# Kernel tuning notes

Measured on AMD Instinct MI355X. Metric: run time of the kernel, lower is better.

## Reference

```python
import jax, jax.numpy as jnp
import numpy as np

N_NODES = 100000
N_EDGES = 3200000
D = 256


def setup_inputs() -> dict:
    key = jax.random.key(0)
    ks = jax.random.split(key, 8)
    ego_embeddings = jax.random.normal(ks[0], (N_NODES, D), dtype=jnp.float32) * 0.1
    edge_vals = jax.random.uniform(ks[1], (N_EDGES,), dtype=jnp.float32) / 32.0  # ~normalized adjacency
    W1 = jax.random.normal(ks[2], (D, D), dtype=jnp.float32) * (1.0 / np.sqrt(D))
    b1 = jnp.zeros((D,), dtype=jnp.float32)
    W2 = jax.random.normal(ks[3], (D, D), dtype=jnp.float32) * (1.0 / np.sqrt(D))
    b2 = jnp.zeros((D,), dtype=jnp.float32)
    edge_rows = jax.random.randint(ks[4], (N_EDGES,), 0, N_NODES, dtype=jnp.int32)
    edge_cols = jax.random.randint(ks[5], (N_EDGES,), 0, N_NODES, dtype=jnp.int32)
    return {"ego_embeddings": ego_embeddings, "edge_vals": edge_vals,
            "W1": W1, "b1": b1, "W2": W2, "b2": b2,
            "edge_rows": edge_rows, "edge_cols": edge_cols}


def reference(ego_embeddings, edge_vals, W1, b1, W2, b2, edge_rows, edge_cols):
    # SpMM: side = A_in @ ego  (A_in in COO: rows, cols, vals)
    n = ego_embeddings.shape[0]
    gathered = ego_embeddings[edge_cols] * edge_vals[:, None]      # [E, D]
    side = jax.ops.segment_sum(gathered, edge_rows, num_segments=n)  # [N, D]
    # bi-interaction aggregator
    sum_emb = jax.nn.leaky_relu((ego_embeddings + side) @ W1.T + b1, negative_slope=0.01)
    bi_emb = jax.nn.leaky_relu((ego_embeddings * side) @ W2.T + b2, negative_slope=0.01)
    # dropout p=0.0 -> identity
    return sum_emb + bi_emb
```

## Files before the change

### kernel.cpp

```cpp
#include <hip/hip_runtime.h>
#include <hip/hip_fp16.h>
#include <stdint.h>

#define D 256
#define CHSH 13

typedef __attribute__((ext_vector_type(8))) short short8;
typedef __attribute__((ext_vector_type(4))) float floatx4;

__device__ __forceinline__ ushort f2bf(float f) {
    union { float f; uint32_t u; } v; v.f = f;
    uint32_t u = v.u;
    u += 0x7fffu + ((u >> 16) & 1u);
    return (ushort)(u >> 16);
}
__device__ __forceinline__ float bf2f(ushort h) {
    union { uint32_t u; float f; } v; v.u = ((uint32_t)h) << 16;
    return v.f;
}


__global__ void k_hist(const int* __restrict__ er, const int* __restrict__ ec,
                       int* __restrict__ bp, int E, int NCH) {
    int e = blockIdx.x * 256 + threadIdx.x;
    if (e >= E) return;
    atomicAdd(&bp[er[e] * NCH + (ec[e] >> CHSH)], 1);
}

__global__ void k_red(const int* __restrict__ bp, int* __restrict__ part, int nb) {
    __shared__ int s[256];
    int t = threadIdx.x;
    int base = blockIdx.x * 1024 + t * 4;
    int v = 0;
#pragma unroll
    for (int j = 0; j < 4; ++j) if (base + j < nb) v += bp[base + j];
    s[t] = v; __syncthreads();
    for (int off = 128; off; off >>= 1) {
        if (t < off) s[t] += s[t + off];
        __syncthreads();
    }
    if (t == 0) part[blockIdx.x] = s[0];
}

__global__ __launch_bounds__(1024) void k_scanpart(int* __restrict__ part, int np) {
    __shared__ int s[1024];
    int t = threadIdx.x;
    int p0 = (2 * t < np) ? part[2 * t] : 0;
    int p1 = (2 * t + 1 < np) ? part[2 * t + 1] : 0;
    int v = p0 + p1;
    s[t] = v; __syncthreads();
    for (int off = 1; off < 1024; off <<= 1) {
        int x = (t >= off) ? s[t - off] : 0;
        __syncthreads();
        s[t] += x;
        __syncthreads();
    }
    int excl = s[t] - v;
    if (2 * t < np) part[2 * t] = excl;
    if (2 * t + 1 < np) part[2 * t + 1] = excl + p0;
}

__global__ void k_scan3(int* __restrict__ bp, const int* __restrict__ part, int nb) {
    __shared__ int s[256];
    int t = threadIdx.x;
    int base = blockIdx.x * 1024 + t * 4;
    int d0 = 0, d1 = 0, d2 = 0, d3 = 0;
    if (base     < nb) d0 = bp[base];
    if (base + 1 < nb) d1 = bp[base + 1];
    if (base + 2 < nb) d2 = bp[base + 2];
    if (base + 3 < nb) d3 = bp[base + 3];
    int sum = d0 + d1 + d2 + d3;
    s[t] = sum; __syncthreads();
    for (int off = 1; off < 256; off <<= 1) {
        int x = (t >= off) ? s[t - off] : 0;
        __syncthreads();
        s[t] += x;
        __syncthreads();
    }
    int run = part[blockIdx.x] + s[t] - sum;
    if (base     < nb) bp[base]     = run; run += d0;
    if (base + 1 < nb) bp[base + 1] = run; run += d1;
    if (base + 2 < nb) bp[base + 2] = run; run += d2;
    if (base + 3 < nb) bp[base + 3] = run;
}

__global__ void k_scatter(const int* __restrict__ er, const int* __restrict__ ec,
                          const float* __restrict__ ev, int* __restrict__ bp,
                          uint32_t* __restrict__ csr, int E, int NCH) {
    int e = blockIdx.x * 256 + threadIdx.x;
    if (e >= E) return;
    int col = ec[e];
    int p = atomicAdd(&bp[er[e] * NCH + (col >> CHSH)], 1);
    ushort hb = __half_as_ushort(__float2half_rn(ev[e]));
    csr[p] = ((uint32_t)col << 15) | (uint32_t)hb;
}

__global__ void k_cvt(const float4* __restrict__ ego, ushort4* __restrict__ ego_bf,
                      const float4* __restrict__ W1, const float4* __restrict__ W2,
                      ushort4* __restrict__ W1b, ushort4* __restrict__ W2b, int n4) {
    int i = blockIdx.x * 256 + threadIdx.x;
    const float4* src;
    ushort4* dst;
    if (i < n4) { src = ego + i; dst = ego_bf + i; }
    else {
        int j = i - n4;
        if (j >= 32768) return;
        int k = j & 16383;
        src = ((j < 16384) ? W1 : W2) + k;
        dst = ((j < 16384) ? W1b : W2b) + k;
    }
    float4 f = *src;
    ushort4 u;
    u.x = f2bf(f.x); u.y = f2bf(f.y); u.z = f2bf(f.z); u.w = f2bf(f.w);
    *dst = u;
}

__global__ void k_spmm(const ushort* __restrict__ ego_bf, const int* __restrict__ bp,
                       const uint32_t* __restrict__ csr,
                       ushort* __restrict__ X1, ushort* __restrict__ X2, int n, int NCH) {
    int gtid = blockIdx.x * 256 + threadIdx.x;
    int node = gtid >> 6;
    int lane = gtid & 63;
    if (node >= n) return;
    int beg = (node == 0) ? 0 : bp[node * NCH - 1];
    int end = bp[(node + 1) * NCH - 1];
    int d0 = lane * 4;
    float a0 = 0.f, a1 = 0.f, a2 = 0.f, a3 = 0.f;
    int e = beg;
    for (; e + 8 <= end; e += 8) {
        uint32_t w[8];
#pragma unroll
        for (int j = 0; j < 8; ++j) w[j] = csr[e + j];
        ushort4 u[8];
#pragma unroll
        for (int j = 0; j < 8; ++j)
            u[j] = *(const ushort4*)(ego_bf + (size_t)(w[j] >> 15) * D + d0);
#pragma unroll
        for (int j = 0; j < 8; ++j) {
            float v = __half2float(__ushort_as_half((ushort)(w[j] & 0x7fff)));
            a0 += v * bf2f(u[j].x);
            a1 += v * bf2f(u[j].y);
            a2 += v * bf2f(u[j].z);
            a3 += v * bf2f(u[j].w);
        }
    }
    for (; e < end; ++e) {
        uint32_t w = csr[e];
        float v = __half2float(__ushort_as_half((ushort)(w & 0x7fff)));
        ushort4 u = *(const ushort4*)(ego_bf + (size_t)(w >> 15) * D + d0);
        a0 += v * bf2f(u.x);
        a1 += v * bf2f(u.y);
        a2 += v * bf2f(u.z);
        a3 += v * bf2f(u.w);
    }
    ushort4 eg = *(const ushort4*)(ego_bf + (size_t)node * D + d0);
    float e0 = bf2f(eg.x), e1 = bf2f(eg.y), e2 = bf2f(eg.z), e3 = bf2f(eg.w);
    ushort4 o1, o2;
    o1.x = f2bf(e0 + a0); o2.x = f2bf(e0 * a0);
    o1.y = f2bf(e1 + a1); o2.y = f2bf(e1 * a1);
    o1.z = f2bf(e2 + a2); o2.z = f2bf(e2 * a2);
    o1.w = f2bf(e3 + a3); o2.w = f2bf(e3 * a3);
    *(ushort4*)(X1 + (size_t)node * D + d0) = o1;
    *(ushort4*)(X2 + (size_t)node * D + d0) = o2;
}

__global__ __launch_bounds__(256) void k_gemm(
        const ushort* __restrict__ X1, const ushort* __restrict__ X2,
        const ushort* __restrict__ W1b, const ushort* __restrict__ W2b,
        const float* __restrict__ b1, const float* __restrict__ b2,
        float* __restrict__ out, int n) {
    int lane = threadIdx.x & 63;
    int w = threadIdx.x >> 6;
    int l16 = lane & 15, quad = lane >> 4;
    int row0 = blockIdx.x * 64;
    int colw = w * 64;

    floatx4 acc1[4][4], acc2[4][4];
#pragma unroll
    for (int i = 0; i < 4; ++i)
#pragma unroll
        for (int j = 0; j < 4; ++j) { acc1[i][j] = (floatx4)0.f; acc2[i][j] = (floatx4)0.f; }

    for (int kk = 0; kk < D; kk += 32) {
        short8 a[4], b[4];
#pragma unroll
        for (int mt = 0; mt < 4; ++mt)
            a[mt] = *(const short8*)(X1 + (size_t)(row0 + mt * 16 + l16) * D + kk + quad * 8);
#pragma unroll
        for (int nt = 0; nt < 4; ++nt)
            b[nt] = *(const short8*)(W1b + (size_t)(colw + nt * 16 + l16) * D + kk + quad * 8);
#pragma unroll
        for (int mt = 0; mt < 4; ++mt)
#pragma unroll
            for (int nt = 0; nt < 4; ++nt)
                acc1[mt][nt] = __builtin_amdgcn_mfma_f32_16x16x32_bf16(a[mt], b[nt], acc1[mt][nt], 0, 0, 0);
    }
    for (int kk = 0; kk < D; kk += 32) {
        short8 a[4], b[4];
#pragma unroll
        for (int mt = 0; mt < 4; ++mt)
            a[mt] = *(const short8*)(X2 + (size_t)(row0 + mt * 16 + l16) * D + kk + quad * 8);
#pragma unroll
        for (int nt = 0; nt < 4; ++nt)
            b[nt] = *(const short8*)(W2b + (size_t)(colw + nt * 16 + l16) * D + kk + quad * 8);
#pragma unroll
        for (int mt = 0; mt < 4; ++mt)
#pragma unroll
            for (int nt = 0; nt < 4; ++nt)
                acc2[mt][nt] = __builtin_amdgcn_mfma_f32_16x16x32_bf16(a[mt], b[nt], acc2[mt][nt], 0, 0, 0);
    }

#pragma unroll
    for (int nt = 0; nt < 4; ++nt) {
        int col = colw + nt * 16 + l16;
        float bb1 = b1[col], bb2 = b2[col];
#pragma unroll
        for (int mt = 0; mt < 4; ++mt) {
            int row = row0 + mt * 16 + quad * 4;
#pragma unroll
            for (int r = 0; r < 4; ++r) {
                if (row + r < n) {
                    float v1 = acc1[mt][nt][r] + bb1;
                    v1 = v1 > 0.f ? v1 : 0.01f * v1;
                    float v2 = acc2[mt][nt][r] + bb2;
                    v2 = v2 > 0.f ? v2 : 0.01f * v2;
                    out[(size_t)(row + r) * D + col] = v1 + v2;
                }
            }
        }
    }
}

extern "C" void kernel_launch(void* const* d_in, const int* in_sizes, int n_in,
                              void* d_out, int out_size, void* d_ws, size_t ws_size,
                              hipStream_t stream) {
    const float* ego   = (const float*)d_in[0];
    const float* evals = (const float*)d_in[1];
    const float* W1    = (const float*)d_in[2];
    const float* b1    = (const float*)d_in[3];
    const float* W2    = (const float*)d_in[4];
    const float* b2    = (const float*)d_in[5];
    const int* erows   = (const int*)d_in[6];
    const int* ecols   = (const int*)d_in[7];
    float* out = (float*)d_out;

    int n = in_sizes[0] / D;
    int E = in_sizes[1];
    int npad = (n + 63) & ~63;
    int NCH = (n + (1 << CHSH) - 1) >> CHSH;
    int nb = n * NCH;
    int np = (nb + 1023) / 1024;

    char* p = (char*)d_ws;
    auto alloc = [&](size_t bytes) {
        char* q = p;
        p += (bytes + 511) & ~(size_t)511;
        return q;
    };
    ushort* ego_bf = (ushort*)alloc((size_t)n * D * 2);
    ushort* X1     = (ushort*)alloc((size_t)npad * D * 2);
    ushort* X2     = (ushort*)alloc((size_t)npad * D * 2);
    ushort* W1b    = (ushort*)alloc((size_t)D * D * 2);
    ushort* W2b    = (ushort*)alloc((size_t)D * D * 2);
    int* bp        = (int*)alloc((size_t)nb * 4);
    int* part      = (int*)alloc((size_t)np * 4);
    uint32_t* csr  = (uint32_t*)alloc((size_t)E * 4);

    hipMemsetAsync(bp, 0, (size_t)nb * 4, stream);
    k_hist<<<(E + 255) / 256, 256, 0, stream>>>(erows, ecols, bp, E, NCH);
    k_red<<<np, 256, 0, stream>>>(bp, part, nb);
    k_scanpart<<<1, 1024, 0, stream>>>(part, np);
    k_scan3<<<np, 256, 0, stream>>>(bp, part, nb);
    k_scatter<<<(E + 255) / 256, 256, 0, stream>>>(erows, ecols, evals, bp, csr, E, NCH);

    int n4 = n * (D / 4);
    k_cvt<<<(n4 + 32768 + 255) / 256, 256, 0, stream>>>((const float4*)ego, (ushort4*)ego_bf,
                                                        (const float4*)W1, (const float4*)W2,
                                                        (ushort4*)W1b, (ushort4*)W2b, n4);

    k_spmm<<<(n * 64 + 255) / 256, 256, 0, stream>>>(ego_bf, bp, csr, X1, X2, n, NCH);

    k_gemm<<<npad / 64, 256, 0, stream>>>(X1, X2, W1b, W2b, b1, b2, out, n);
}
```

Before: 893.2 us.

## Replace global fine-grained bucket sort with two-level 64-row bin sort for CSR

The CSR build no longer runs a global histogram plus a three-kernel scan over n*NCH buckets (about 1.3M counters). Edges are first binned into groups of 64 rows using a shared-memory histogram and a single-block scan. Each bin is then locally sorted by (row, column-chunk) in shared memory, which also produces the row pointers. This cuts global atomics contention and the large scan passes. In exchange it adds an 8-byte intermediate record pass, which reuses the X2 buffer as scratch, and the scan assumes at most 2048 bins.

```diff
diff --git a/kernel.cpp b/kernel.cpp
--- a/kernel.cpp
+++ b/kernel.cpp
@@ -20,33 +20,31 @@
 }
 
 
-__global__ void k_hist(const int* __restrict__ er, const int* __restrict__ ec,
-                       int* __restrict__ bp, int E, int NCH) {
-    int e = blockIdx.x * 256 + threadIdx.x;
-    if (e >= E) return;
-    atomicAdd(&bp[er[e] * NCH + (ec[e] >> CHSH)], 1);
-}
-
-__global__ void k_red(const int* __restrict__ bp, int* __restrict__ part, int nb) {
-    __shared__ int s[256];
+__global__ __launch_bounds__(1024) void k_hist0(const int* __restrict__ er,
+                                                int* __restrict__ cc, int E, int NB) {
+    __shared__ int h[2048];
     int t = threadIdx.x;
-    int base = blockIdx.x * 1024 + t * 4;
-    int v = 0;
-#pragma unroll
-    for (int j = 0; j < 4; ++j) if (base + j < nb) v += bp[base + j];
-    s[t] = v; __syncthreads();
-    for (int off = 128; off; off >>= 1) {
-        if (t < off) s[t] += s[t + off];
-        __syncthreads();
-    }
-    if (t == 0) part[blockIdx.x] = s[0];
-}
-
-__global__ __launch_bounds__(1024) void k_scanpart(int* __restrict__ part, int np) {
+    h[t] = 0; h[t + 1024] = 0;
+    __syncthreads();
+    int base = blockIdx.x * 32768;
+    for (int i = t; i < 32768; i += 1024) {
+        int e = base + i;
+        if (e < E) atomicAdd(&h[er[e] >> 6], 1);
+    }
+    __syncthreads();
+    int v = h[t];
+    if (t < NB && v) atomicAdd(&cc[t], v);
+    v = h[t + 1024];
+    if (t + 1024 < NB && v) atomicAdd(&cc[t + 1024], v);
+}
+
+__global__ __launch_bounds__(1024) void k_scan0(const int* __restrict__ cc,
+                                                int* __restrict__ cbase, int* __restrict__ cursor,
+                                                int* __restrict__ rowp, int NB, int E, int n) {
     __shared__ int s[1024];
     int t = threadIdx.x;
-    int p0 = (2 * t < np) ? part[2 * t] : 0;
-    int p1 = (2 * t + 1 < np) ? part[2 * t + 1] : 0;
+    int p0 = (2 * t < NB) ? cc[2 * t] : 0;
+    int p1 = (2 * t + 1 < NB) ? cc[2 * t + 1] : 0;
     int v = p0 + p1;
     s[t] = v; __syncthreads();
     for (int off = 1; off < 1024; off <<= 1) {
@@ -56,43 +54,60 @@
         __syncthreads();
     }
     int excl = s[t] - v;
-    if (2 * t < np) part[2 * t] = excl;
-    if (2 * t + 1 < np) part[2 * t + 1] = excl + p0;
-}
-
-__global__ void k_scan3(int* __restrict__ bp, const int* __restrict__ part, int nb) {
-    __shared__ int s[256];
-    int t = threadIdx.x;
-    int base = blockIdx.x * 1024 + t * 4;
-    int d0 = 0, d1 = 0, d2 = 0, d3 = 0;
-    if (base     < nb) d0 = bp[base];
-    if (base + 1 < nb) d1 = bp[base + 1];
-    if (base + 2 < nb) d2 = bp[base + 2];
-    if (base + 3 < nb) d3 = bp[base + 3];
-    int sum = d0 + d1 + d2 + d3;
-    s[t] = sum; __syncthreads();
-    for (int off = 1; off < 256; off <<= 1) {
-        int x = (t >= off) ? s[t - off] : 0;
-        __syncthreads();
-        s[t] += x;
-        __syncthreads();
-    }
-    int run = part[blockIdx.x] + s[t] - sum;
-    if (base     < nb) bp[base]     = run; run += d0;
-    if (base + 1 < nb) bp[base + 1] = run; run += d1;
-    if (base + 2 < nb) bp[base + 2] = run; run += d2;
-    if (base + 3 < nb) bp[base + 3] = run;
-}
-
-__global__ void k_scatter(const int* __restrict__ er, const int* __restrict__ ec,
-                          const float* __restrict__ ev, int* __restrict__ bp,
-                          uint32_t* __restrict__ csr, int E, int NCH) {
+    if (2 * t < NB)     { cbase[2 * t] = excl;          cursor[2 * t] = excl; }
+    if (2 * t + 1 < NB) { cbase[2 * t + 1] = excl + p0; cursor[2 * t + 1] = excl + p0; }
+    if (t == 0) { cbase[NB] = E; rowp[n] = E; }
+}
+
+__global__ void k_scatterA(const int* __restrict__ er, const int* __restrict__ ec,
+                           const float* __restrict__ ev, int* __restrict__ cursor,
+                           uint2* __restrict__ rec, int E, int NCH) {
     int e = blockIdx.x * 256 + threadIdx.x;
     if (e >= E) return;
-    int col = ec[e];
-    int p = atomicAdd(&bp[er[e] * NCH + (col >> CHSH)], 1);
+    int r = er[e], c = ec[e];
+    int p = atomicAdd(&cursor[r >> 6], 1);
     ushort hb = __half_as_ushort(__float2half_rn(ev[e]));
-    csr[p] = ((uint32_t)col << 15) | (uint32_t)hb;
+    rec[p] = make_uint2((unsigned)((r & 63) * NCH + (c >> CHSH)),
+                        ((uint32_t)c << 15) | (uint32_t)hb);
+}
+
+__global__ __launch_bounds__(256) void k_binB(const uint2* __restrict__ rec,
+                                              const int* __restrict__ cbase,
+                                              uint32_t* __restrict__ csr,
+                                              int* __restrict__ rowp, int NCH, int n) {
+    __shared__ int h[1024];
+    __shared__ int ws[256];
+    int t = threadIdx.x, b = blockIdx.x;
+    int base = cbase[b], cnt = cbase[b + 1] - base;
+    h[t] = 0; h[t + 256] = 0; h[t + 512] = 0; h[t + 768] = 0;
+    __syncthreads();
+    for (int i = t; i < cnt; i += 256) atomicAdd(&h[rec[base + i].x], 1);
+    __syncthreads();
+    int c0 = h[4 * t], c1 = h[4 * t + 1], c2 = h[4 * t + 2], c3 = h[4 * t + 3];
+    int s = c0 + c1 + c2 + c3;
+    ws[t] = s; __syncthreads();
+    for (int off = 1; off < 256; off <<= 1) {
+        int x = (t >= off) ? ws[t - off] : 0;
+        __syncthreads();
+        ws[t] += x;
+        __syncthreads();
+    }
+    int run = ws[t] - s;
+    h[4 * t] = run; run += c0;
+    h[4 * t + 1] = run; run += c1;
+    h[4 * t + 2] = run; run += c2;
+    h[4 * t + 3] = run;
+    __syncthreads();
+    if (t < 64) {
+        int grow = b * 64 + t;
+        if (grow < n) rowp[grow] = base + h[t * NCH];
+    }
+    __syncthreads();
+    for (int i = t; i < cnt; i += 256) {
+        uint2 r = rec[base + i];
+        int pos = base + atomicAdd(&h[r.x], 1);
+        csr[pos] = r.y;
+    }
 }
 
 __global__ void k_cvt(const float4* __restrict__ ego, ushort4* __restrict__ ego_bf,
@@ -115,15 +130,14 @@
     *dst = u;
 }
 
-__global__ void k_spmm(const ushort* __restrict__ ego_bf, const int* __restrict__ bp,
+__global__ void k_spmm(const ushort* __restrict__ ego_bf, const int* __restrict__ rowp,
                        const uint32_t* __restrict__ csr,
-                       ushort* __restrict__ X1, ushort* __restrict__ X2, int n, int NCH) {
+                       ushort* __restrict__ X1, ushort* __restrict__ X2, int n) {
     int gtid = blockIdx.x * 256 + threadIdx.x;
     int node = gtid >> 6;
     int lane = gtid & 63;
     if (node >= n) return;
-    int beg = (node == 0) ? 0 : bp[node * NCH - 1];
-    int end = bp[(node + 1) * NCH - 1];
+    int beg = rowp[node], end = rowp[node + 1];
     int d0 = lane * 4;
     float a0 = 0.f, a1 = 0.f, a2 = 0.f, a3 = 0.f;
     int e = beg;
@@ -248,8 +262,7 @@
     int E = in_sizes[1];
     int npad = (n + 63) & ~63;
     int NCH = (n + (1 << CHSH) - 1) >> CHSH;
-    int nb = n * NCH;
-    int np = (nb + 1023) / 1024;
+    int NB = (n + 63) >> 6;
 
     char* p = (char*)d_ws;
     auto alloc = [&](size_t bytes) {
@@ -262,23 +275,25 @@
     ushort* X2     = (ushort*)alloc((size_t)npad * D * 2);
     ushort* W1b    = (ushort*)alloc((size_t)D * D * 2);
     ushort* W2b    = (ushort*)alloc((size_t)D * D * 2);
-    int* bp        = (int*)alloc((size_t)nb * 4);
-    int* part      = (int*)alloc((size_t)np * 4);
     uint32_t* csr  = (uint32_t*)alloc((size_t)E * 4);
-
-    hipMemsetAsync(bp, 0, (size_t)nb * 4, stream);
-    k_hist<<<(E + 255) / 256, 256, 0, stream>>>(erows, ecols, bp, E, NCH);
-    k_red<<<np, 256, 0, stream>>>(bp, part, nb);
-    k_scanpart<<<1, 1024, 0, stream>>>(part, np);
-    k_scan3<<<np, 256, 0, stream>>>(bp, part, nb);
-    k_scatter<<<(E + 255) / 256, 256, 0, stream>>>(erows, ecols, evals, bp, csr, E, NCH);
+    int* cc        = (int*)alloc((size_t)(NB + 1) * 4);
+    int* cbase     = (int*)alloc((size_t)(NB + 1) * 4);
+    int* cursor    = (int*)alloc((size_t)NB * 4);
+    int* rowp      = (int*)alloc((size_t)(n + 1) * 4);
+    uint2* recA    = (uint2*)X2;
+
+    hipMemsetAsync(cc, 0, (size_t)(NB + 1) * 4, stream);
+    k_hist0<<<(E + 32767) / 32768, 1024, 0, stream>>>(erows, cc, E, NB);
+    k_scan0<<<1, 1024, 0, stream>>>(cc, cbase, cursor, rowp, NB, E, n);
+    k_scatterA<<<(E + 255) / 256, 256, 0, stream>>>(erows, ecols, evals, cursor, recA, E, NCH);
+    k_binB<<<NB, 256, 0, stream>>>(recA, cbase, csr, rowp, NCH, n);
 
     int n4 = n * (D / 4);
     k_cvt<<<(n4 + 32768 + 255) / 256, 256, 0, stream>>>((const float4*)ego, (ushort4*)ego_bf,
                                                         (const float4*)W1, (const float4*)W2,
                                                         (ushort4*)W1b, (ushort4*)W2b, n4);
 
-    k_spmm<<<(n * 64 + 255) / 256, 256, 0, stream>>>(ego_bf, bp, csr, X1, X2, n, NCH);
+    k_spmm<<<(n * 64 + 255) / 256, 256, 0, stream>>>(ego_bf, rowp, csr, X1, X2, n);
 
     k_gemm<<<npad / 64, 256, 0, stream>>>(X1, X2, W1b, W2b, b1, b2, out, n);
 }
```

New measurement: 1.069 ms. 19.7% more time.
